# Kernel optimization log

Hardware: AMD Instinct MI355X
Metric: run time of the kernel (lower is better)

The kernel has to match this reference:

```python
import jax, jax.numpy as jnp
import numpy as np

DIM = 2048
N_HEADS = 32
N_KV_HEADS = 4
HEAD_DIM = DIM // N_HEADS  # 64


def _rope_tables(T, head_dim, dtype):
    inv_freq = 1.0 / (10000.0 ** (jnp.arange(0, head_dim, 2, dtype=jnp.float32) / head_dim))
    t = jnp.arange(T, dtype=jnp.float32)
    freqs = jnp.einsum('i,j->ij', t, inv_freq)           # [T, head_dim/2]
    emb = jnp.concatenate([freqs, freqs], axis=-1)        # [T, head_dim]
    return jnp.cos(emb).astype(dtype), jnp.sin(emb).astype(dtype)


def _rotate_half(x):
    d = x.shape[-1] // 2
    return jnp.concatenate([-x[..., d:], x[..., :d]], axis=-1)


def setup_inputs() -> dict:
    key = jax.random.key(0)
    kx, kq, kk, kv, ko = jax.random.split(key, 5)
    s = 1.0 / np.sqrt(DIM)
    return {
        'x': jax.random.normal(kx, (2, 2048, DIM), dtype=jnp.float32),
        'wq': jax.random.normal(kq, (DIM, DIM), dtype=jnp.float32) * s,
        'wk': jax.random.normal(kk, (DIM, DIM // 8), dtype=jnp.float32) * s,
        'wv': jax.random.normal(kv, (DIM, DIM // 8), dtype=jnp.float32) * s,
        'wo': jax.random.normal(ko, (DIM, DIM), dtype=jnp.float32) * s,
    }


def reference(x, wq, wk, wv, wo):
    B, T, C = x.shape
    q = (x @ wq).reshape(B, T, N_HEADS, HEAD_DIM).transpose(0, 2, 1, 3)      # [B,H,T,D]
    k = (x @ wk).reshape(B, T, N_KV_HEADS, HEAD_DIM).transpose(0, 2, 1, 3)   # [B,Hkv,T,D]
    v = (x @ wv).reshape(B, T, N_KV_HEADS, HEAD_DIM).transpose(0, 2, 1, 3)

    cos, sin = _rope_tables(T, HEAD_DIM, x.dtype)  # [T,D]
    q = q * cos + _rotate_half(q) * sin
    k = k * cos + _rotate_half(k) * sin

    rep = N_HEADS // N_KV_HEADS
    k = jnp.repeat(k, rep, axis=1)  # [B,H,T,D]
    v = jnp.repeat(v, rep, axis=1)

    scale = 1.0 / np.sqrt(HEAD_DIM)
    scores = jnp.einsum('bhqd,bhkd->bhqk', q, k) * scale
    causal = jnp.tril(jnp.ones((T, T), dtype=bool))
    scores = jnp.where(causal, scores, jnp.finfo(scores.dtype).min)
    attn = jax.nn.softmax(scores, axis=-1)
    out = jnp.einsum('bhqk,bhkd->bhqd', attn, v)
    out = out.transpose(0, 2, 1, 3).reshape(B, T, C)
    return out @ wo
```

## Files before the change

kernel.cpp:

```cpp
#include <hip/hip_runtime.h>
#include <hip/hip_bf16.h>
#include <stdint.h>

#define DIM 2048
#define TSEQ 2048
#define BATCH 2
#define NH 32
#define NKV 4
#define HD 64
#define MROWS (BATCH*TSEQ)
#define NQKV 2560

typedef __attribute__((ext_vector_type(4))) float f32x4;
typedef __attribute__((ext_vector_type(8))) __bf16 bf16x8;
typedef unsigned short ushort_t;

#define GLDS16(g, l) __builtin_amdgcn_global_load_lds( \
    (const __attribute__((address_space(1))) void*)(g), \
    (__attribute__((address_space(3))) void*)(l), 16, 0, 0)

__device__ __forceinline__ float bflo2f(unsigned int w) {
  union { unsigned int i; float f; } c; c.i = w << 16; return c.f;
}
__device__ __forceinline__ unsigned short f2bf(float f) {
  union { float f; unsigned int i; } c; c.f = f;
  unsigned int x = c.i;
  x += 0x7fffu + ((x >> 16) & 1u);
  return (unsigned short)(x >> 16);
}
__device__ __forceinline__ unsigned short f2bf_fast(float f) {
  union { float f; unsigned int i; } c; c.f = f;
  return (unsigned short)((c.i + 0x8000u) >> 16);
}

__global__ void cast_bf16_k(const float* __restrict__ in, ushort_t* __restrict__ out, int n4) {
  const int i = blockIdx.x * 256 + threadIdx.x;
  if (i >= n4) return;
  const float4 v = ((const float4*)in)[i];
  uint2 p;
  p.x = (unsigned int)f2bf(v.x) | ((unsigned int)f2bf(v.y) << 16);
  p.y = (unsigned int)f2bf(v.z) | ((unsigned int)f2bf(v.w) << 16);
  ((uint2*)out)[i] = p;
}

__global__ void transpose_cast_all(const float* __restrict__ wq, const float* __restrict__ wk,
                                   const float* __restrict__ wv, const float* __restrict__ wo,
                                   ushort_t* __restrict__ wtq, ushort_t* __restrict__ woT) {
  __shared__ float tile[32][33];
  const int by = blockIdx.y;
  const float* src; ushort_t* dst; int N, bnb;
  if (by < 64)      { src = wq; dst = wtq;                    N = DIM; bnb = by; }
  else if (by < 72) { src = wk; dst = wtq + (long)DIM  * DIM; N = 256; bnb = by - 64; }
  else if (by < 80) { src = wv; dst = wtq + (long)2304 * DIM; N = 256; bnb = by - 72; }
  else              { src = wo; dst = woT;                    N = DIM; bnb = by - 80; }
  const int bk = blockIdx.x * 32;
  const int bn = bnb * 32;
  const int tx = threadIdx.x & 31;
  const int ty = threadIdx.x >> 5;
#pragma unroll
  for (int p = 0; p < 4; p++) {
    const int r = ty + p * 8;
    tile[r][tx] = src[(long)(bk + r) * N + bn + tx];
  }
  __syncthreads();
#pragma unroll
  for (int p = 0; p < 4; p++) {
    const int r = ty + p * 8;
    dst[(long)(bn + r) * DIM + bk + tx] = f2bf(tile[tx][r]);
  }
}

#define LOG1E4_D32 0.2878231366242557f
#define QSCALE 0.1803368801111243f

__global__ void rope_tab_k(float2* __restrict__ tab) {
  const int i = blockIdx.x * 256 + threadIdx.x;
  const int t = i >> 5, d = i & 31;
  const float ang = (float)t * __expf(-(float)d * LOG1E4_D32);
  float s_, c_;
  __sincosf(ang, &s_, &c_);
  tab[i] = make_float2(c_, s_);
}

template<int EPI>
__global__ __launch_bounds__(256, 2) void gemm_bt(
    const ushort_t* __restrict__ A, const ushort_t* __restrict__ BT,
    int M, int N, int K,
    float* __restrict__ Cf, ushort_t* __restrict__ Cq,
    ushort_t* __restrict__ Ck, ushort_t* __restrict__ Cv,
    const float2* __restrict__ tab)
{
  __shared__ __align__(16) ushort_t As[128][64];
  __shared__ __align__(16) ushort_t Bs[128][64];
  const int tid  = threadIdx.x;
  const int lane = tid & 63;
  const int wid  = tid >> 6;
  const int wm   = wid >> 1, wn = wid & 1;
  const int l8   = lane >> 3;
  const int c8   = (lane & 7) * 8;
  const long abase = (long)blockIdx.x * 128 * K;
  const long bbase = (long)blockIdx.y * 128 * K;
  const int rsel = lane & 15;
  const int koff = (lane >> 4) * 8;
  f32x4 acc[4][4] = {};

  for (int k0 = 0; k0 < K; k0 += 64) {
    __syncthreads();
#pragma unroll
    for (int i = 0; i < 4; i++) {
      const int r0 = wid * 32 + i * 8;
      GLDS16(&A [abase + (long)(r0 + l8) * K + k0 + c8], &As[r0][0]);
      GLDS16(&BT[bbase + (long)(r0 + l8) * K + k0 + c8], &Bs[r0][0]);
    }
    __syncthreads();
#pragma unroll
    for (int kk = 0; kk < 64; kk += 32) {
      bf16x8 af[4], bfr[4];
#pragma unroll
      for (int m = 0; m < 4; m++) af[m]  = *(const bf16x8*)(&As[wm*64 + m*16 + rsel][kk + koff]);
#pragma unroll
      for (int n = 0; n < 4; n++) bfr[n] = *(const bf16x8*)(&Bs[wn*64 + n*16 + rsel][kk + koff]);
#pragma unroll
      for (int m = 0; m < 4; m++)
#pragma unroll
        for (int n = 0; n < 4; n++)
          acc[m][n] = __builtin_amdgcn_mfma_f32_16x16x32_bf16(af[m], bfr[n], acc[m][n], 0, 0, 0);
    }
  }

  const int rbase = blockIdx.x * 128 + wm * 64 + (lane >> 4) * 4;
  const int l15e  = lane & 15;

  if (EPI == 1) {
    const int cbase = blockIdx.y * 128 + wn * 64 + l15e;
#pragma unroll
    for (int m = 0; m < 4; m++)
#pragma unroll
      for (int n = 0; n < 4; n++) {
        const int gn = cbase + n * 16;
#pragma unroll
        for (int j = 0; j < 4; j++)
          Cf[(long)(rbase + m * 16 + j) * N + gn] = acc[m][n][j];
      }
  } else {
    const int colbase = blockIdx.y * 128 + wn * 64;
    if (colbase >= DIM + 256) {
#pragma unroll
      for (int m = 0; m < 4; m++)
#pragma unroll
        for (int n = 0; n < 4; n++) {
          const int x = colbase + n * 16 + l15e - DIM;
          const int hkv = (x >> 6) & 3;
          const int d = x & 63;
#pragma unroll
          for (int j = 0; j < 4; j++) {
            const int gm = rbase + m * 16 + j;
            const int b = gm >> 11;
            const int t = gm & (TSEQ - 1);
            Cv[((long)(b * NKV + hkv) * HD + d) * TSEQ + t] = f2bf(acc[m][n][j]);
          }
        }
    } else {
      const bool isQ = (colbase < DIM);
      const int hkv = (colbase - DIM) >> 6;
#pragma unroll
      for (int m = 0; m < 4; m++) {
#pragma unroll
        for (int j = 0; j < 4; j++) {
          const int gm = rbase + m * 16 + j;
          const int t = gm & (TSEQ - 1);
          const int b = gm >> 11;
          const float2 cs0 = tab[t * 32 + l15e];
          const float2 cs1 = tab[t * 32 + 16 + l15e];
          const float v0 = acc[m][0][j], v1 = acc[m][1][j];
          const float v2 = acc[m][2][j], v3 = acc[m][3][j];
          const float r0 = v0 * cs0.x - v2 * cs0.y;
          const float r2 = v2 * cs0.x + v0 * cs0.y;
          const float r1 = v1 * cs1.x - v3 * cs1.y;
          const float r3 = v3 * cs1.x + v1 * cs1.y;
          if (isQ) {
            const long base = (long)gm * DIM + colbase + l15e;
            Cq[base]      = f2bf(r0 * QSCALE);
            Cq[base + 16] = f2bf(r1 * QSCALE);
            Cq[base + 32] = f2bf(r2 * QSCALE);
            Cq[base + 48] = f2bf(r3 * QSCALE);
          } else {
            const long base = ((long)(b * NKV + hkv) * TSEQ + t) * HD + l15e;
            Ck[base]      = f2bf(r0);
            Ck[base + 16] = f2bf(r1);
            Ck[base + 32] = f2bf(r2);
            Ck[base + 48] = f2bf(r3);
          }
        }
      }
    }
  }
}

__global__ __launch_bounds__(512, 6) void attn_mfma(
    const ushort_t* __restrict__ q, const ushort_t* __restrict__ k,
    const ushort_t* __restrict__ vt, ushort_t* __restrict__ o)
{
  __shared__ __align__(16) ushort_t Ks[2][64][64];
  __shared__ __align__(16) ushort_t Vs[2][64][64];

  const int tid  = threadIdx.x;
  const int lane = tid & 63;
  const int wid  = tid >> 6;
  const int l15  = lane & 15;
  const int lg   = lane >> 4;
  const int od   = lg & 1;
  const int hi   = lg >> 1;
  const int sw   = l15 & 7;

  const int bh  = blockIdx.x & 63;
  const int qt  = (TSEQ / 128 - 1) - (blockIdx.x >> 6);
  const int h   = bh & (NH - 1);
  const int b   = bh >> 5;
  const int hkv = h >> 3;
  const int qbase = qt * 128;
  const int qw0   = qbase + wid * 16;

  bf16x8 qf[2];
  {
    const ushort_t* qp = q + ((long)(b * TSEQ) + qw0 + l15) * DIM + h * 64 + lg * 8;
    qf[0] = *(const bf16x8*)(qp);
    qf[1] = *(const bf16x8*)(qp + 32);
  }

  const ushort_t* kb_ = k  + (long)(b * NKV + hkv) * TSEQ * HD;
  const ushort_t* vb_ = vt + (long)(b * NKV + hkv) * HD * TSEQ;

  float l_c = 0.f;
  f32x4 o_[4] = {};

  const int srow = tid >> 3;
  const int sgc  = (tid & 7) * 8;
  const int slc  = (((tid & 7) ^ (srow & 7))) * 8;

  const int gv0 = ((0 + 2 * od + hi) ^ sw) * 8;
  const int gv1 = ((4 + 2 * od + hi) ^ sw) * 8;

  const int nkv = 2 * (qt + 1);

  *(uint4*)(&Ks[0][srow][slc]) = *(const uint4*)(&kb_[(long)srow * HD + sgc]);
  *(uint4*)(&Vs[0][srow][slc]) = *(const uint4*)(&vb_[(long)srow * TSEQ + sgc]);
  int cur = 0;

  for (int kbv = 0; kbv < nkv; kbv++) {
    const int kb0 = kbv * 64;
    const bool pf = (kbv + 1 < nkv);
    uint4 kr = {}, vr = {};
    if (pf) {
      kr = *(const uint4*)(&kb_[(long)(kb0 + 64 + srow) * HD + sgc]);
      vr = *(const uint4*)(&vb_[(long)srow * TSEQ + kb0 + 64 + sgc]);
    }
    asm volatile("s_waitcnt lgkmcnt(0)\n\ts_barrier" ::: "memory");

    if (kb0 <= qw0 + 15) {
      f32x4 st[4] = {};
#pragma unroll
      for (int kt = 0; kt < 4; kt++) {
#pragma unroll
        for (int c = 0; c < 2; c++) {
          const bf16x8 kf = *(const bf16x8*)(&Ks[cur][kt * 16 + l15][((4*c + lg) ^ sw) * 8]);
          st[kt] = __builtin_amdgcn_mfma_f32_16x16x32_bf16(kf, qf[c], st[kt], 0, 0, 0);
        }
      }

      if (kb0 + 63 > qw0) {
        const int qg = qw0 + l15;
#pragma unroll
        for (int kt = 0; kt < 4; kt++) {
          const int kg0 = kb0 + kt * 16 + lg * 4;
#pragma unroll
          for (int j = 0; j < 4; j++) {
            if (kg0 + j > qg) st[kt][j] = -1e30f;
          }
        }
      }

      unsigned int u00, u01, u10, u11, u20, u21, u30, u31;
#define PACK_KT(KT, UA, UB) { \
        const float p0 = exp2f(st[KT][0]); \
        const float p1 = exp2f(st[KT][1]); \
        const float p2 = exp2f(st[KT][2]); \
        const float p3 = exp2f(st[KT][3]); \
        l_c += (p0 + p1) + (p2 + p3); \
        asm("v_cvt_pk_bf16_f32 %0, %1, %2" : "=v"(UA) : "v"(p0), "v"(p1)); \
        asm("v_cvt_pk_bf16_f32 %0, %1, %2" : "=v"(UB) : "v"(p2), "v"(p3)); \
      }
      PACK_KT(0, u00, u01)
      PACK_KT(1, u10, u11)
      PACK_KT(2, u20, u21)
      PACK_KT(3, u30, u31)
#undef PACK_KT

      const unsigned int r00 = __shfl_xor((int)(od ? u00 : u10), 16, 64);
      const unsigned int r01 = __shfl_xor((int)(od ? u01 : u11), 16, 64);
      const unsigned int r10 = __shfl_xor((int)(od ? u20 : u30), 16, 64);
      const unsigned int r11 = __shfl_xor((int)(od ? u21 : u31), 16, 64);
      union { unsigned int u[4]; bf16x8 v; } T0, T1;
      T0.u[0] = od ? r00 : u00;  T0.u[1] = od ? r01 : u01;
      T0.u[2] = od ? u10 : r00;  T0.u[3] = od ? u11 : r01;
      T1.u[0] = od ? r10 : u20;  T1.u[1] = od ? r11 : u21;
      T1.u[2] = od ? u30 : r10;  T1.u[3] = od ? u31 : r11;

#pragma unroll
      for (int nt = 0; nt < 4; nt++) {
        const bf16x8 vf0 = *(const bf16x8*)(&Vs[cur][nt * 16 + l15][gv0]);
        o_[nt] = __builtin_amdgcn_mfma_f32_16x16x32_bf16(T0.v, vf0, o_[nt], 0, 0, 0);
      }
#pragma unroll
      for (int nt = 0; nt < 4; nt++) {
        const bf16x8 vf1 = *(const bf16x8*)(&Vs[cur][nt * 16 + l15][gv1]);
        o_[nt] = __builtin_amdgcn_mfma_f32_16x16x32_bf16(T1.v, vf1, o_[nt], 0, 0, 0);
      }
    }

    if (pf) {
      *(uint4*)(&Ks[cur ^ 1][srow][slc]) = kr;
      *(uint4*)(&Vs[cur ^ 1][srow][slc]) = vr;
    }
    cur ^= 1;
  }

  l_c += __shfl_xor(l_c, 16, 64);
  l_c += __shfl_xor(l_c, 32, 64);
  const long orow = (long)(b * TSEQ) + qw0;
#pragma unroll
  for (int j = 0; j < 4; j++) {
    const float inv = 1.f / __shfl(l_c, (lane & 48) | (lg * 4 + j), 64);
#pragma unroll
    for (int nt = 0; nt < 4; nt++)
      o[(orow + lg * 4 + j) * DIM + h * 64 + nt * 16 + l15] = f2bf_fast(o_[nt][j] * inv);
  }
}

extern "C" void kernel_launch(void* const* d_in, const int* in_sizes, int n_in,
                              void* d_out, int out_size, void* d_ws, size_t ws_size,
                              hipStream_t stream) {
  const float* x  = (const float*)d_in[0];
  const float* wq = (const float*)d_in[1];
  const float* wk = (const float*)d_in[2];
  const float* wv = (const float*)d_in[3];
  const float* wo = (const float*)d_in[4];
  float* out = (float*)d_out;

  ushort_t* ws = (ushort_t*)d_ws;
  const long NXB = (long)MROWS * DIM;
  ushort_t* xb   = ws;
  ushort_t* wtq  = xb  + NXB;
  ushort_t* woT  = wtq + (long)NQKV * DIM;
  ushort_t* qws  = woT + (long)DIM * DIM;
  ushort_t* kws  = qws + NXB;
  ushort_t* vtws = kws + (long)BATCH * NKV * TSEQ * HD;
  ushort_t* aws  = vtws + (long)BATCH * NKV * TSEQ * HD;
  float2*   tab  = (float2*)(aws + NXB);

  cast_bf16_k<<<(int)(NXB / 1024), 256, 0, stream>>>(x, xb, (int)(NXB / 4));
  transpose_cast_all<<<dim3(64, 144), 256, 0, stream>>>(wq, wk, wv, wo, wtq, woT);
  rope_tab_k<<<256, 256, 0, stream>>>(tab);

  gemm_bt<0><<<dim3(32, 20), 256, 0, stream>>>(xb, wtq, MROWS, NQKV, DIM,
                                               nullptr, qws, kws, vtws, tab);

  attn_mfma<<<BATCH * NH * (TSEQ / 128), 512, 0, stream>>>(qws, kws, vtws, aws);

  gemm_bt<1><<<dim3(32, 16), 256, 0, stream>>>(aws, woT, MROWS, DIM, DIM,
                                               out, nullptr, nullptr, nullptr, nullptr);
}
```

Measured before the change: 199.4 us.

## Double attention query tile per block and pack V-transpose stores

The attention kernel now processes 256 query rows per block, with 32 per wave split into two 16-row halves, so each K/V tile staged in shared memory serves twice as many queries. The grid halves and launch bounds drop to 4 waves-per-SIMD occupancy to fit the doubled accumulators. The V-transposed epilogue of the QKV GEMM now packs four bf16 values into one 8-byte store instead of four scalar stores. The trade is fewer blocks, which can worsen causal load imbalance, and higher register pressure.

```diff
diff --git a/kernel.cpp b/kernel.cpp
--- a/kernel.cpp
+++ b/kernel.cpp
@@ -146,20 +146,21 @@
     const int colbase = blockIdx.y * 128 + wn * 64;
     if (colbase >= DIM + 256) {
 #pragma unroll
-      for (int m = 0; m < 4; m++)
+      for (int m = 0; m < 4; m++) {
+        const int gm0 = rbase + m * 16;
+        const int b = gm0 >> 11;
+        const int t = gm0 & (TSEQ - 1);
 #pragma unroll
         for (int n = 0; n < 4; n++) {
           const int x = colbase + n * 16 + l15e - DIM;
           const int hkv = (x >> 6) & 3;
           const int d = x & 63;
-#pragma unroll
-          for (int j = 0; j < 4; j++) {
-            const int gm = rbase + m * 16 + j;
-            const int b = gm >> 11;
-            const int t = gm & (TSEQ - 1);
-            Cv[((long)(b * NKV + hkv) * HD + d) * TSEQ + t] = f2bf(acc[m][n][j]);
-          }
-        }
+          uint2 pk;
+          pk.x = (unsigned int)f2bf(acc[m][n][0]) | ((unsigned int)f2bf(acc[m][n][1]) << 16);
+          pk.y = (unsigned int)f2bf(acc[m][n][2]) | ((unsigned int)f2bf(acc[m][n][3]) << 16);
+          *(uint2*)(&Cv[((long)(b * NKV + hkv) * HD + d) * TSEQ + t]) = pk;
+        }
+      }
     } else {
       const bool isQ = (colbase < DIM);
       const int hkv = (colbase - DIM) >> 6;
@@ -197,7 +198,7 @@
   }
 }
 
-__global__ __launch_bounds__(512, 6) void attn_mfma(
+__global__ __launch_bounds__(512, 4) void attn_mfma(
     const ushort_t* __restrict__ q, const ushort_t* __restrict__ k,
     const ushort_t* __restrict__ vt, ushort_t* __restrict__ o)
 {
@@ -214,25 +215,26 @@
   const int sw   = l15 & 7;
 
   const int bh  = blockIdx.x & 63;
-  const int qt  = (TSEQ / 128 - 1) - (blockIdx.x >> 6);
+  const int qt  = (TSEQ / 256 - 1) - (blockIdx.x >> 6);
   const int h   = bh & (NH - 1);
   const int b   = bh >> 5;
   const int hkv = h >> 3;
-  const int qbase = qt * 128;
-  const int qw0   = qbase + wid * 16;
-
-  bf16x8 qf[2];
-  {
-    const ushort_t* qp = q + ((long)(b * TSEQ) + qw0 + l15) * DIM + h * 64 + lg * 8;
-    qf[0] = *(const bf16x8*)(qp);
-    qf[1] = *(const bf16x8*)(qp + 32);
+  const int qbase = qt * 256;
+  const int qw0   = qbase + wid * 32;
+
+  bf16x8 qf[2][2];
+#pragma unroll
+  for (int hh = 0; hh < 2; hh++) {
+    const ushort_t* qp = q + ((long)(b * TSEQ) + qw0 + hh * 16 + l15) * DIM + h * 64 + lg * 8;
+    qf[hh][0] = *(const bf16x8*)(qp);
+    qf[hh][1] = *(const bf16x8*)(qp + 32);
   }
 
   const ushort_t* kb_ = k  + (long)(b * NKV + hkv) * TSEQ * HD;
   const ushort_t* vb_ = vt + (long)(b * NKV + hkv) * HD * TSEQ;
 
-  float l_c = 0.f;
-  f32x4 o_[4] = {};
+  float l_c[2] = {0.f, 0.f};
+  f32x4 o_[2][4] = {};
 
   const int srow = tid >> 3;
   const int sgc  = (tid & 7) * 8;
@@ -241,7 +243,7 @@
   const int gv0 = ((0 + 2 * od + hi) ^ sw) * 8;
   const int gv1 = ((4 + 2 * od + hi) ^ sw) * 8;
 
-  const int nkv = 2 * (qt + 1);
+  const int nkv = 4 * (qt + 1);
 
   *(uint4*)(&Ks[0][srow][slc]) = *(const uint4*)(&kb_[(long)srow * HD + sgc]);
   *(uint4*)(&Vs[0][srow][slc]) = *(const uint4*)(&vb_[(long)srow * TSEQ + sgc]);
@@ -257,64 +259,68 @@
     }
     asm volatile("s_waitcnt lgkmcnt(0)\n\ts_barrier" ::: "memory");
 
-    if (kb0 <= qw0 + 15) {
-      f32x4 st[4] = {};
-#pragma unroll
-      for (int kt = 0; kt < 4; kt++) {
-#pragma unroll
-        for (int c = 0; c < 2; c++) {
-          const bf16x8 kf = *(const bf16x8*)(&Ks[cur][kt * 16 + l15][((4*c + lg) ^ sw) * 8]);
-          st[kt] = __builtin_amdgcn_mfma_f32_16x16x32_bf16(kf, qf[c], st[kt], 0, 0, 0);
-        }
-      }
-
-      if (kb0 + 63 > qw0) {
-        const int qg = qw0 + l15;
+#pragma unroll
+    for (int hh = 0; hh < 2; hh++) {
+      const int qh0 = qw0 + hh * 16;
+      if (kb0 <= qh0 + 15) {
+        f32x4 st[4] = {};
 #pragma unroll
         for (int kt = 0; kt < 4; kt++) {
-          const int kg0 = kb0 + kt * 16 + lg * 4;
-#pragma unroll
-          for (int j = 0; j < 4; j++) {
-            if (kg0 + j > qg) st[kt][j] = -1e30f;
+#pragma unroll
+          for (int c = 0; c < 2; c++) {
+            const bf16x8 kf = *(const bf16x8*)(&Ks[cur][kt * 16 + l15][((4*c + lg) ^ sw) * 8]);
+            st[kt] = __builtin_amdgcn_mfma_f32_16x16x32_bf16(kf, qf[hh][c], st[kt], 0, 0, 0);
           }
         }
-      }
-
-      unsigned int u00, u01, u10, u11, u20, u21, u30, u31;
+
+        if (kb0 + 63 > qh0) {
+          const int qg = qh0 + l15;
+#pragma unroll
+          for (int kt = 0; kt < 4; kt++) {
+            const int kg0 = kb0 + kt * 16 + lg * 4;
+#pragma unroll
+            for (int j = 0; j < 4; j++) {
+              if (kg0 + j > qg) st[kt][j] = -1e30f;
+            }
+          }
+        }
+
+        unsigned int u00, u01, u10, u11, u20, u21, u30, u31;
 #define PACK_KT(KT, UA, UB) { \
-        const float p0 = exp2f(st[KT][0]); \
-        const float p1 = exp2f(st[KT][1]); \
-        const float p2 = exp2f(st[KT][2]); \
-        const float p3 = exp2f(st[KT][3]); \
-        l_c += (p0 + p1) + (p2 + p3); \
-        asm("v_cvt_pk_bf16_f32 %0, %1, %2" : "=v"(UA) : "v"(p0), "v"(p1)); \
-        asm("v_cvt_pk_bf16_f32 %0, %1, %2" : "=v"(UB) : "v"(p2), "v"(p3)); \
-      }
-      PACK_KT(0, u00, u01)
-      PACK_KT(1, u10, u11)
-      PACK_KT(2, u20, u21)
-      PACK_KT(3, u30, u31)
+          const float p0 = exp2f(st[KT][0]); \
+          const float p1 = exp2f(st[KT][1]); \
+          const float p2 = exp2f(st[KT][2]); \
+          const float p3 = exp2f(st[KT][3]); \
+          l_c[hh] += (p0 + p1) + (p2 + p3); \
+          asm("v_cvt_pk_bf16_f32 %0, %1, %2" : "=v"(UA) : "v"(p0), "v"(p1)); \
+          asm("v_cvt_pk_bf16_f32 %0, %1, %2" : "=v"(UB) : "v"(p2), "v"(p3)); \
+        }
+        PACK_KT(0, u00, u01)
+        PACK_KT(1, u10, u11)
+        PACK_KT(2, u20, u21)
+        PACK_KT(3, u30, u31)
 #undef PACK_KT
 
-      const unsigned int r00 = __shfl_xor((int)(od ? u00 : u10), 16, 64);
-      const unsigned int r01 = __shfl_xor((int)(od ? u01 : u11), 16, 64);
-      const unsigned int r10 = __shfl_xor((int)(od ? u20 : u30), 16, 64);
-      const unsigned int r11 = __shfl_xor((int)(od ? u21 : u31), 16, 64);
-      union { unsigned int u[4]; bf16x8 v; } T0, T1;
-      T0.u[0] = od ? r00 : u00;  T0.u[1] = od ? r01 : u01;
-      T0.u[2] = od ? u10 : r00;  T0.u[3] = od ? u11 : r01;
-      T1.u[0] = od ? r10 : u20;  T1.u[1] = od ? r11 : u21;
-      T1.u[2] = od ? u30 : r10;  T1.u[3] = od ? u31 : r11;
-
-#pragma unroll
-      for (int nt = 0; nt < 4; nt++) {
-        const bf16x8 vf0 = *(const bf16x8*)(&Vs[cur][nt * 16 + l15][gv0]);
-        o_[nt] = __builtin_amdgcn_mfma_f32_16x16x32_bf16(T0.v, vf0, o_[nt], 0, 0, 0);
-      }
-#pragma unroll
-      for (int nt = 0; nt < 4; nt++) {
-        const bf16x8 vf1 = *(const bf16x8*)(&Vs[cur][nt * 16 + l15][gv1]);
-        o_[nt] = __builtin_amdgcn_mfma_f32_16x16x32_bf16(T1.v, vf1, o_[nt], 0, 0, 0);
+        const unsigned int r00 = __shfl_xor((int)(od ? u00 : u10), 16, 64);
+        const unsigned int r01 = __shfl_xor((int)(od ? u01 : u11), 16, 64);
+        const unsigned int r10 = __shfl_xor((int)(od ? u20 : u30), 16, 64);
+        const unsigned int r11 = __shfl_xor((int)(od ? u21 : u31), 16, 64);
+        union { unsigned int u[4]; bf16x8 v; } T0, T1;
+        T0.u[0] = od ? r00 : u00;  T0.u[1] = od ? r01 : u01;
+        T0.u[2] = od ? u10 : r00;  T0.u[3] = od ? u11 : r01;
+        T1.u[0] = od ? r10 : u20;  T1.u[1] = od ? r11 : u21;
+        T1.u[2] = od ? u30 : r10;  T1.u[3] = od ? u31 : r11;
+
+#pragma unroll
+        for (int nt = 0; nt < 4; nt++) {
+          const bf16x8 vf0 = *(const bf16x8*)(&Vs[cur][nt * 16 + l15][gv0]);
+          o_[hh][nt] = __builtin_amdgcn_mfma_f32_16x16x32_bf16(T0.v, vf0, o_[hh][nt], 0, 0, 0);
+        }
+#pragma unroll
+        for (int nt = 0; nt < 4; nt++) {
+          const bf16x8 vf1 = *(const bf16x8*)(&Vs[cur][nt * 16 + l15][gv1]);
+          o_[hh][nt] = __builtin_amdgcn_mfma_f32_16x16x32_bf16(T1.v, vf1, o_[hh][nt], 0, 0, 0);
+        }
       }
     }
 
@@ -325,15 +331,19 @@
     cur ^= 1;
   }
 
-  l_c += __shfl_xor(l_c, 16, 64);
-  l_c += __shfl_xor(l_c, 32, 64);
-  const long orow = (long)(b * TSEQ) + qw0;
-#pragma unroll
-  for (int j = 0; j < 4; j++) {
-    const float inv = 1.f / __shfl(l_c, (lane & 48) | (lg * 4 + j), 64);
-#pragma unroll
-    for (int nt = 0; nt < 4; nt++)
-      o[(orow + lg * 4 + j) * DIM + h * 64 + nt * 16 + l15] = f2bf_fast(o_[nt][j] * inv);
+#pragma unroll
+  for (int hh = 0; hh < 2; hh++) {
+    float lc = l_c[hh];
+    lc += __shfl_xor(lc, 16, 64);
+    lc += __shfl_xor(lc, 32, 64);
+    const long orow = (long)(b * TSEQ) + qw0 + hh * 16;
+#pragma unroll
+    for (int j = 0; j < 4; j++) {
+      const float inv = 1.f / __shfl(lc, (lane & 48) | (lg * 4 + j), 64);
+#pragma unroll
+      for (int nt = 0; nt < 4; nt++)
+        o[(orow + lg * 4 + j) * DIM + h * 64 + nt * 16 + l15] = f2bf_fast(o_[hh][nt][j] * inv);
+    }
   }
 }
 
@@ -365,7 +375,7 @@
   gemm_bt<0><<<dim3(32, 20), 256, 0, stream>>>(xb, wtq, MROWS, NQKV, DIM,
                                                nullptr, qws, kws, vtws, tab);
 
-  attn_mfma<<<BATCH * NH * (TSEQ / 128), 512, 0, stream>>>(qws, kws, vtws, aws);
+  attn_mfma<<<BATCH * NH * (TSEQ / 256), 512, 0, stream>>>(qws, kws, vtws, aws);
 
   gemm_bt<1><<<dim3(32, 16), 256, 0, stream>>>(aws, woT, MROWS, DIM, DIM,
                                                out, nullptr, nullptr, nullptr, nullptr);
```

Result: slower. 210.9 us (+5.8%).
